# Optimization experiments

Measured on AMD Instinct MI355X. Metric: run time of the kernel, lower is better.

Reference implementation:

```python
import jax, jax.numpy as jnp
import numpy as np

D_MODEL = 2048
D_COMPARE = 2048
D_MEMORY = 2048
N_HEADS = 16
KV_HEADS = 4
KV_REPEAT = N_HEADS // KV_HEADS          # 4
C_HD = D_COMPARE // N_HEADS              # 128 compare head dim
M_HD = D_MEMORY // N_HEADS               # 128 memory head dim
TOTAL_OUT = D_COMPARE + KV_HEADS * C_HD + KV_HEADS * M_HD  # 3072


def setup_inputs() -> dict:
    key = jax.random.key(0)
    ks = jax.random.split(key, 5)
    b, t = 2, 2048
    x = jax.random.normal(ks[0], (b, t, D_MODEL), dtype=jnp.float32)
    s_in = 1.0 / np.sqrt(D_MODEL)
    s_out = 1.0 / np.sqrt(D_MEMORY)
    in_w = jax.random.uniform(ks[1], (TOTAL_OUT, D_MODEL), jnp.float32, -s_in, s_in)
    in_b = jax.random.uniform(ks[2], (TOTAL_OUT,), jnp.float32, -s_in, s_in)
    out_w = jax.random.uniform(ks[3], (D_MODEL, D_MEMORY), jnp.float32, -s_out, s_out)
    out_b = jax.random.uniform(ks[4], (D_MODEL,), jnp.float32, -s_out, s_out)
    return {"x": x, "in_w": in_w, "in_b": in_b, "out_w": out_w, "out_b": out_b}


def reference(x, in_w, in_b, out_w, out_b):
    b, t, _ = x.shape
    packed = jnp.einsum("btd,od->bto", x, in_w) + in_b          # [b,t,TOTAL_OUT]
    q, k, v = jnp.split(packed, [D_COMPARE, D_COMPARE + KV_HEADS * C_HD], axis=-1)
    # q: [b, kv, rep, t, hd] -- head h maps to kv group h // KV_REPEAT
    # (torch repeat_interleave on KV head dim == grouped reshape of q heads)
    q = q.reshape(b, t, KV_HEADS, KV_REPEAT, C_HD).transpose(0, 2, 3, 1, 4)
    k = k.reshape(b, t, KV_HEADS, C_HD).transpose(0, 2, 1, 3)   # [b,kv,t,hd]
    v = v.reshape(b, t, KV_HEADS, M_HD).transpose(0, 2, 1, 3)   # [b,kv,t,mhd]
    scale = 1.0 / np.sqrt(C_HD)
    scores = jnp.einsum("bgrqd,bgkd->bgrqk", q, k) * scale      # [b,kv,rep,t,t]
    attn = jax.nn.softmax(scores, axis=-1)
    y = jnp.einsum("bgrqk,bgkd->bgrqd", attn, v)                # [b,kv,rep,t,mhd]
    y = y.transpose(0, 3, 1, 2, 4).reshape(b, t, D_MEMORY)      # heads back in order
    return jnp.einsum("btm,dm->btd", y, out_w) + out_b
```

## Files before the change

kernel.cpp:

```cpp
#include <hip/hip_runtime.h>
#include <hip/hip_bf16.h>
#include <stdint.h>

#define DEV __device__ __forceinline__

typedef __attribute__((ext_vector_type(8))) short bf16x8;
typedef __attribute__((ext_vector_type(4))) float f32x4;
typedef __attribute__((ext_vector_type(16))) float f32x16;

DEV unsigned short f2bf(float f) {
  unsigned u = __builtin_bit_cast(unsigned, f);
  unsigned r = u + 0x7FFF + ((u >> 16) & 1);
  return (unsigned short)(r >> 16);
}

DEV unsigned short f2bfh(float f) {
  __bf16 h = (__bf16)f;
  return __builtin_bit_cast(unsigned short, h);
}

typedef __attribute__((address_space(1))) void gvoid;
typedef __attribute__((address_space(3))) void lvoid;

DEV void g2l16(const void* g, void* l) {
  __builtin_amdgcn_global_load_lds((gvoid*)g, (lvoid*)l, 16, 0, 0);
}

#define MFMA16(a, b, c) __builtin_amdgcn_mfma_f32_16x16x32_bf16(a, b, c, 0, 0, 0)
#define MFMA32(a, b, c) __builtin_amdgcn_mfma_f32_32x32x16_bf16(a, b, c, 0, 0, 0)

__global__ void k_cvt3(const float* __restrict__ x, unsigned short* __restrict__ xo, int nx4,
                       const float* __restrict__ w, unsigned short* __restrict__ wo, int nw4,
                       const float* __restrict__ v, unsigned short* __restrict__ vo, int nv4) {
  int i = blockIdx.x * blockDim.x + threadIdx.x;
  int stride = gridDim.x * blockDim.x;
  int tot = nx4 + nw4 + nv4;
  for (; i < tot; i += stride) {
    const float* src; unsigned short* dst; int j = i;
    if (j < nx4) { src = x; dst = xo; }
    else if ((j -= nx4) < nw4) { src = w; dst = wo; }
    else { j -= nw4; src = v; dst = vo; }
    float4 val = reinterpret_cast<const float4*>(src)[j];
    ushort4 o;
    o.x = f2bf(val.x); o.y = f2bf(val.y); o.z = f2bf(val.z); o.w = f2bf(val.w);
    reinterpret_cast<ushort4*>(dst)[j] = o;
  }
}

template<bool BF16OUT>
__global__ __launch_bounds__(256, 2) void k_gemm(
    const unsigned short* __restrict__ A, const unsigned short* __restrict__ B,
    const float* __restrict__ bias, void* __restrict__ C,
    int M, int N, int K) {
  __shared__ unsigned short As[128 * 32];
  __shared__ unsigned short Bs[128 * 32];
  int tid = threadIdx.x;
  int lane = tid & 63, wid = tid >> 6;
  int bm = blockIdx.y * 128, bn = blockIdx.x * 128;
  int wm = (wid >> 1) * 64, wn = (wid & 1) * 64;
  int row16 = lane & 15, kq = lane >> 4;
  f32x4 acc[4][4] = {};
  int r = tid >> 2, c = (tid & 3) * 8;
  const unsigned short* Ag = A + (size_t)(bm + r) * K + c;
  const unsigned short* Bg = B + (size_t)(bn + r) * K + c;
  for (int k0 = 0; k0 < K; k0 += 32) {
    g2l16(Ag + k0, &As[tid * 8]);
    g2l16(Ag + (size_t)64 * K + k0, &As[2048 + tid * 8]);
    g2l16(Bg + k0, &Bs[tid * 8]);
    g2l16(Bg + (size_t)64 * K + k0, &Bs[2048 + tid * 8]);
    __syncthreads();
    bf16x8 a[4], b[4];
#pragma unroll
    for (int m = 0; m < 4; m++) a[m] = *(const bf16x8*)&As[(wm + m * 16 + row16) * 32 + kq * 8];
#pragma unroll
    for (int n = 0; n < 4; n++) b[n] = *(const bf16x8*)&Bs[(wn + n * 16 + row16) * 32 + kq * 8];
    __builtin_amdgcn_s_setprio(1);
#pragma unroll
    for (int m = 0; m < 4; m++)
#pragma unroll
      for (int n = 0; n < 4; n++)
        acc[m][n] = MFMA16(a[m], b[n], acc[m][n]);
    __builtin_amdgcn_s_setprio(0);
    __syncthreads();
  }
#pragma unroll
  for (int n = 0; n < 4; n++) {
    int col = bn + wn + n * 16 + row16;
    float bv = bias[col];
#pragma unroll
    for (int m = 0; m < 4; m++) {
      int rw = bm + wm + m * 16 + kq * 4;
#pragma unroll
      for (int j = 0; j < 4; j++) {
        float v = acc[m][n][j] + bv;
        if (BF16OUT) ((unsigned short*)C)[(size_t)(rw + j) * N + col] = f2bf(v);
        else         ((float*)C)[(size_t)(rw + j) * N + col] = v;
      }
    }
  }
}

__global__ void k_vt(const unsigned short* __restrict__ packed, unsigned short* __restrict__ vT) {
  __shared__ unsigned short tile[64][136];
  int g = blockIdx.y;
  int b = g >> 2, kv = g & 3;
  int t0 = blockIdx.x * 64;
  int tid = threadIdx.x;
#pragma unroll
  for (int i = 0; i < 4; i++) {
    int tl = i * 16 + (tid >> 4);
    int d0 = (tid & 15) * 8;
    bf16x8 v = *(const bf16x8*)&packed[(size_t)(b * 2048 + t0 + tl) * 3072 + 2560 + kv * 128 + d0];
    *(bf16x8*)&tile[tl][d0] = v;
  }
  __syncthreads();
  int d = tid >> 1, ts = (tid & 1) * 32;
  size_t obase = (size_t)(g * 128 + d) * 2048 + t0 + ts;
#pragma unroll
  for (int j = 0; j < 4; j++) {
    bf16x8 o;
#pragma unroll
    for (int e = 0; e < 8; e++) o[e] = (short)tile[ts + j * 8 + e][d];
    *(bf16x8*)&vT[obase + j * 8] = o;
  }
}

__global__ __launch_bounds__(256, 2) void k_flash(
    const unsigned short* __restrict__ packed,
    const unsigned short* __restrict__ vT,
    unsigned short* __restrict__ Y) {
  __shared__ unsigned short Ks[2][64 * 128];
  __shared__ unsigned short Vs[128 * 64];
  __shared__ unsigned short Ps[4][32 * 64];
  __shared__ float Axc[4][32];
  int tid = threadIdx.x, lane = tid & 63, wid = tid >> 6;
  int l31 = lane & 31, hi = lane >> 5;
  int kx = l31 & 15;
  int vx = l31 & 7;
  int g = blockIdx.x;
  int s8 = g & 7;
  int b = s8 >> 2, kv = s8 & 3;
  int w = g >> 3;
  int h = kv * 4 + (w & 3);
  int qt = w >> 2;
  size_t prow = (size_t)b * 2048;

  unsigned short* Q = &Ks[0][0];
  {
    int rr = tid >> 4;
    int cc = ((tid & 15) ^ rr) * 8;
    const unsigned short* qg = packed + (prow + qt * 128 + rr) * 3072 + h * 128 + cc;
#pragma unroll
    for (int i = 0; i < 8; i++)
      g2l16(qg + (size_t)i * 16 * 3072, &Q[i * 2048 + tid * 8]);
  }
  asm volatile("s_waitcnt vmcnt(0)" ::: "memory");
  __builtin_amdgcn_s_barrier();
  bf16x8 q[8];
  int qrow = wid * 32 + l31;
#pragma unroll
  for (int kc = 0; kc < 8; kc++)
    q[kc] = *(const bf16x8*)&Q[qrow * 128 + (((2 * kc + hi) ^ kx) * 8)];
  asm volatile("s_waitcnt lgkmcnt(0)" ::: "memory");
  __builtin_amdgcn_sched_barrier(0);
  __builtin_amdgcn_s_barrier();

  const unsigned short* kg0 = packed + prow * 3072 + 2048 + kv * 128;
  const unsigned short* vg0 = vT + (size_t)(b * 4 + kv) * 128 * 2048;
  int krr = tid >> 4;
  int kcc = ((tid & 15) ^ krr) * 8;
  int vrr = tid >> 3;
  int vcc = ((tid & 7) ^ (vrr & 7)) * 8;

  auto stageK = [&](int t, int kbuf) {
    const unsigned short* kg = kg0 + (size_t)(t * 64 + krr) * 3072 + kcc;
#pragma unroll
    for (int i = 0; i < 4; i++)
      g2l16(kg + (size_t)i * 16 * 3072, &Ks[kbuf][i * 2048 + tid * 8]);
  };
  auto stageV = [&](int t) {
    const unsigned short* vg = vg0 + (size_t)vrr * 2048 + t * 64 + vcc;
#pragma unroll
    for (int i = 0; i < 4; i++)
      g2l16(vg + (size_t)i * 32 * 2048, &Vs[i * 2048 + tid * 8]);
  };

  stageK(0, 0);
  stageV(0);
  asm volatile("s_waitcnt vmcnt(4)" ::: "memory");
  __builtin_amdgcn_s_barrier();

  f32x16 o[4] = {};
  float mr = -1e30f, lr = 0.f;
  const float sc2 = 0.08838834764831845f * 1.4426950408889634f;

  for (int t = 0; t < 32; t++) {
    int kb = t & 1;
    int tn = t < 31 ? t + 1 : 31;

    f32x16 st[2] = {};
#pragma unroll
    for (int kb2 = 0; kb2 < 2; kb2++) {
      bf16x8 ak[8];
#pragma unroll
      for (int kc = 0; kc < 8; kc++)
        ak[kc] = *(const bf16x8*)&Ks[kb][(kb2 * 32 + l31) * 128 + (((2 * kc + hi) ^ kx) * 8)];
      __builtin_amdgcn_s_setprio(1);
#pragma unroll
      for (int kc = 0; kc < 8; kc++)
        st[kb2] = MFMA32(ak[kc], q[kc], st[kb2]);
      __builtin_amdgcn_s_setprio(0);
    }

    stageK(tn, kb ^ 1);

    float m0 = -1e30f, m1 = -1e30f;
#pragma unroll
    for (int r = 0; r < 16; r += 2) {
      m0 = fmaxf(m0, fmaxf(st[0][r], st[0][r + 1]));
      m1 = fmaxf(m1, fmaxf(st[1][r], st[1][r + 1]));
    }
    float p = fmaxf(m0, m1);
    p = fmaxf(p, __shfl_xor(p, 32));
    p *= sc2;
    if (!__all(p <= mr + 8.f)) {
      float mn = fmaxf(mr, p);
      float al = exp2f(mr - mn);
      mr = mn;
      lr *= al;
      Axc[wid][l31] = al;
      float alo[16];
#pragma unroll
      for (int r = 0; r < 16; r++)
        alo[r] = Axc[wid][(r & 3) + 8 * (r >> 2) + 4 * hi];
#pragma unroll
      for (int db = 0; db < 4; db++)
#pragma unroll
        for (int r = 0; r < 16; r++) o[db][r] *= alo[r];
    }
    float nm = -mr;
    float rs = 0.f;
#pragma unroll
    for (int kb2 = 0; kb2 < 2; kb2++) {
      float s[4];
#pragma unroll
      for (int u = 0; u < 4; u++) {
        st[kb2][4 * u + 0] = exp2f(fmaf(st[kb2][4 * u + 0], sc2, nm));
        st[kb2][4 * u + 1] = exp2f(fmaf(st[kb2][4 * u + 1], sc2, nm));
        st[kb2][4 * u + 2] = exp2f(fmaf(st[kb2][4 * u + 2], sc2, nm));
        st[kb2][4 * u + 3] = exp2f(fmaf(st[kb2][4 * u + 3], sc2, nm));
        s[u] = (st[kb2][4 * u + 0] + st[kb2][4 * u + 1]) +
               (st[kb2][4 * u + 2] + st[kb2][4 * u + 3]);
      }
      rs += (s[0] + s[1]) + (s[2] + s[3]);
    }
    rs += __shfl_xor(rs, 32);
    lr += rs;

#pragma unroll
    for (int kb2 = 0; kb2 < 2; kb2++)
#pragma unroll
      for (int u = 0; u < 4; u++) {
        ushort4 pw;
        pw.x = f2bfh(st[kb2][4 * u + 0]);
        pw.y = f2bfh(st[kb2][4 * u + 1]);
        pw.z = f2bfh(st[kb2][4 * u + 2]);
        pw.w = f2bfh(st[kb2][4 * u + 3]);
        *(ushort4*)&Ps[wid][l31 * 64 + (((u + 4 * kb2) ^ vx) * 8) + hi * 4] = pw;
      }
    bf16x8 pf[4];
#pragma unroll
    for (int ks = 0; ks < 4; ks++)
      pf[ks] = *(const bf16x8*)&Ps[wid][l31 * 64 + (((2 * ks + hi) ^ vx) * 8)];

    asm volatile("s_waitcnt vmcnt(4)" ::: "memory");
    __builtin_amdgcn_s_barrier();

#pragma unroll
    for (int db = 0; db < 4; db++) {
      bf16x8 bv[4];
#pragma unroll
      for (int ks = 0; ks < 4; ks++)
        bv[ks] = *(const bf16x8*)&Vs[(32 * db + l31) * 64 + (((2 * ks + hi) ^ vx) * 8)];
      __builtin_amdgcn_s_setprio(1);
#pragma unroll
      for (int ks = 0; ks < 4; ks++)
        o[db] = MFMA32(pf[ks], bv[ks], o[db]);
      __builtin_amdgcn_s_setprio(0);
    }

    __builtin_amdgcn_s_barrier();
    stageV(tn);
    asm volatile("s_waitcnt vmcnt(4)" ::: "memory");
    __builtin_amdgcn_s_barrier();
  }
  asm volatile("s_waitcnt vmcnt(0)" ::: "memory");

  Axc[wid][l31] = lr;
#pragma unroll
  for (int r = 0; r < 16; r++) {
    int ql = (r & 3) + 8 * (r >> 2) + 4 * hi;
    float inv = 1.f / Axc[wid][ql];
    size_t orow = prow + (size_t)qt * 128 + wid * 32 + ql;
#pragma unroll
    for (int db = 0; db < 4; db++)
      Y[orow * 2048 + h * 128 + db * 32 + l31] = f2bfh(o[db][r] * inv);
  }
}

extern "C" void kernel_launch(void* const* d_in, const int* in_sizes, int n_in,
                              void* d_out, int out_size, void* d_ws, size_t ws_size,
                              hipStream_t stream) {
  const float* x     = (const float*)d_in[0];
  const float* in_w  = (const float*)d_in[1];
  const float* in_b  = (const float*)d_in[2];
  const float* out_w = (const float*)d_in[3];
  const float* out_b = (const float*)d_in[4];
  float* out = (float*)d_out;

  unsigned short* xb     = (unsigned short*)d_ws;
  unsigned short* wb     = xb + 8388608;
  unsigned short* owb    = wb + 6291456;
  unsigned short* packed = owb + 4194304;
  unsigned short* vt     = packed + 12582912;
  unsigned short* y      = vt + 2097152;

  k_cvt3<<<dim3(2048), dim3(256), 0, stream>>>(x, xb, 8388608 / 4,
                                               in_w, wb, 6291456 / 4,
                                               out_w, owb, 4194304 / 4);

  k_gemm<true><<<dim3(24, 32), dim3(256), 0, stream>>>(xb, wb, in_b, packed, 4096, 3072, 2048);
  k_vt<<<dim3(32, 8), dim3(256), 0, stream>>>(packed, vt);
  k_flash<<<dim3(512), dim3(256), 0, stream>>>(packed, vt, y);
  k_gemm<false><<<dim3(16, 32), dim3(256), 0, stream>>>(y, owb, out_b, out, 4096, 2048, 2048);
}
```

Baseline: 225.2 us.

## Keep P in registers via permlane swap, double-buffer V, compute row sums with MFMA

The P matrix is converted to bf16 with packed converts and rearranged across lanes with v_permlane32_swap, so it no longer goes through an LDS round trip. V gets a second LDS buffer, and K and V for the next tile are both prefetched at the top of each iteration, which cuts the per-iteration barriers from three to one. Row sums are now accumulated by MFMA against a ones vector instead of scalar adds and shuffles. In exchange it uses more LDS and spends extra MFMA work on the sums, and the row sums now come from bf16-rounded P values.

```diff
diff --git a/kernel.cpp b/kernel.cpp
--- a/kernel.cpp
+++ b/kernel.cpp
@@ -7,6 +7,7 @@
 typedef __attribute__((ext_vector_type(8))) short bf16x8;
 typedef __attribute__((ext_vector_type(4))) float f32x4;
 typedef __attribute__((ext_vector_type(16))) float f32x16;
+typedef __attribute__((ext_vector_type(4))) unsigned u32x4;
 
 DEV unsigned short f2bf(float f) {
   unsigned u = __builtin_bit_cast(unsigned, f);
@@ -17,6 +18,16 @@
 DEV unsigned short f2bfh(float f) {
   __bf16 h = (__bf16)f;
   return __builtin_bit_cast(unsigned short, h);
+}
+
+DEV unsigned cvtpk(float lo, float hi) {
+  unsigned r;
+  asm("v_cvt_pk_bf16_f32 %0, %1, %2" : "=v"(r) : "v"(lo), "v"(hi));
+  return r;
+}
+
+DEV void plswap(unsigned &a, unsigned &b) {
+  asm("v_permlane32_swap_b32 %0, %1" : "+v"(a), "+v"(b));
 }
 
 typedef __attribute__((address_space(1))) void gvoid;
@@ -130,8 +141,7 @@
     const unsigned short* __restrict__ vT,
     unsigned short* __restrict__ Y) {
   __shared__ unsigned short Ks[2][64 * 128];
-  __shared__ unsigned short Vs[128 * 64];
-  __shared__ unsigned short Ps[4][32 * 64];
+  __shared__ unsigned short Vs[2][128 * 64];
   __shared__ float Axc[4][32];
   int tid = threadIdx.x, lane = tid & 63, wid = tid >> 6;
   int l31 = lane & 31, hi = lane >> 5;
@@ -172,31 +182,38 @@
   int vrr = tid >> 3;
   int vcc = ((tid & 7) ^ (vrr & 7)) * 8;
 
-  auto stageK = [&](int t, int kbuf) {
+  auto stageK = [&](int t, int buf) {
     const unsigned short* kg = kg0 + (size_t)(t * 64 + krr) * 3072 + kcc;
 #pragma unroll
     for (int i = 0; i < 4; i++)
-      g2l16(kg + (size_t)i * 16 * 3072, &Ks[kbuf][i * 2048 + tid * 8]);
+      g2l16(kg + (size_t)i * 16 * 3072, &Ks[buf][i * 2048 + tid * 8]);
   };
-  auto stageV = [&](int t) {
+  auto stageV = [&](int t, int buf) {
     const unsigned short* vg = vg0 + (size_t)vrr * 2048 + t * 64 + vcc;
 #pragma unroll
     for (int i = 0; i < 4; i++)
-      g2l16(vg + (size_t)i * 32 * 2048, &Vs[i * 2048 + tid * 8]);
+      g2l16(vg + (size_t)i * 32 * 2048, &Vs[buf][i * 2048 + tid * 8]);
   };
 
   stageK(0, 0);
-  stageV(0);
-  asm volatile("s_waitcnt vmcnt(4)" ::: "memory");
+  stageV(0, 0);
+  asm volatile("s_waitcnt vmcnt(0)" ::: "memory");
   __builtin_amdgcn_s_barrier();
 
   f32x16 o[4] = {};
-  float mr = -1e30f, lr = 0.f;
+  f32x16 ls = {};
+  float mr = -1e30f;
   const float sc2 = 0.08838834764831845f * 1.4426950408889634f;
+  bf16x8 ones;
+#pragma unroll
+  for (int e = 0; e < 8; e++) ones[e] = (short)0x3F80;
 
   for (int t = 0; t < 32; t++) {
-    int kb = t & 1;
+    int buf = t & 1;
     int tn = t < 31 ? t + 1 : 31;
+
+    stageK(tn, buf ^ 1);
+    stageV(tn, buf ^ 1);
 
     f32x16 st[2] = {};
 #pragma unroll
@@ -204,15 +221,13 @@
       bf16x8 ak[8];
 #pragma unroll
       for (int kc = 0; kc < 8; kc++)
-        ak[kc] = *(const bf16x8*)&Ks[kb][(kb2 * 32 + l31) * 128 + (((2 * kc + hi) ^ kx) * 8)];
+        ak[kc] = *(const bf16x8*)&Ks[buf][(kb2 * 32 + l31) * 128 + (((2 * kc + hi) ^ kx) * 8)];
       __builtin_amdgcn_s_setprio(1);
 #pragma unroll
       for (int kc = 0; kc < 8; kc++)
         st[kb2] = MFMA32(ak[kc], q[kc], st[kb2]);
       __builtin_amdgcn_s_setprio(0);
     }
-
-    stageK(tn, kb ^ 1);
 
     float m0 = -1e30f, m1 = -1e30f;
 #pragma unroll
@@ -227,7 +242,6 @@
       float mn = fmaxf(mr, p);
       float al = exp2f(mr - mn);
       mr = mn;
-      lr *= al;
       Axc[wid][l31] = al;
       float alo[16];
 #pragma unroll
@@ -237,70 +251,57 @@
       for (int db = 0; db < 4; db++)
 #pragma unroll
         for (int r = 0; r < 16; r++) o[db][r] *= alo[r];
+#pragma unroll
+      for (int r = 0; r < 16; r++) ls[r] *= alo[r];
     }
     float nm = -mr;
-    float rs = 0.f;
+#pragma unroll
+    for (int kb2 = 0; kb2 < 2; kb2++)
+#pragma unroll
+      for (int r = 0; r < 16; r++)
+        st[kb2][r] = exp2f(fmaf(st[kb2][r], sc2, nm));
+
+    bf16x8 pf[4];
 #pragma unroll
     for (int kb2 = 0; kb2 < 2; kb2++) {
-      float s[4];
-#pragma unroll
-      for (int u = 0; u < 4; u++) {
-        st[kb2][4 * u + 0] = exp2f(fmaf(st[kb2][4 * u + 0], sc2, nm));
-        st[kb2][4 * u + 1] = exp2f(fmaf(st[kb2][4 * u + 1], sc2, nm));
-        st[kb2][4 * u + 2] = exp2f(fmaf(st[kb2][4 * u + 2], sc2, nm));
-        st[kb2][4 * u + 3] = exp2f(fmaf(st[kb2][4 * u + 3], sc2, nm));
-        s[u] = (st[kb2][4 * u + 0] + st[kb2][4 * u + 1]) +
-               (st[kb2][4 * u + 2] + st[kb2][4 * u + 3]);
-      }
-      rs += (s[0] + s[1]) + (s[2] + s[3]);
-    }
-    rs += __shfl_xor(rs, 32);
-    lr += rs;
-
-#pragma unroll
-    for (int kb2 = 0; kb2 < 2; kb2++)
-#pragma unroll
-      for (int u = 0; u < 4; u++) {
-        ushort4 pw;
-        pw.x = f2bfh(st[kb2][4 * u + 0]);
-        pw.y = f2bfh(st[kb2][4 * u + 1]);
-        pw.z = f2bfh(st[kb2][4 * u + 2]);
-        pw.w = f2bfh(st[kb2][4 * u + 3]);
-        *(ushort4*)&Ps[wid][l31 * 64 + (((u + 4 * kb2) ^ vx) * 8) + hi * 4] = pw;
-      }
-    bf16x8 pf[4];
-#pragma unroll
-    for (int ks = 0; ks < 4; ks++)
-      pf[ks] = *(const bf16x8*)&Ps[wid][l31 * 64 + (((2 * ks + hi) ^ vx) * 8)];
-
-    asm volatile("s_waitcnt vmcnt(4)" ::: "memory");
-    __builtin_amdgcn_s_barrier();
+      unsigned E0 = cvtpk(st[kb2][0],  st[kb2][1]);
+      unsigned E1 = cvtpk(st[kb2][2],  st[kb2][3]);
+      unsigned E2 = cvtpk(st[kb2][4],  st[kb2][5]);
+      unsigned E3 = cvtpk(st[kb2][6],  st[kb2][7]);
+      unsigned E4 = cvtpk(st[kb2][8],  st[kb2][9]);
+      unsigned E5 = cvtpk(st[kb2][10], st[kb2][11]);
+      unsigned E6 = cvtpk(st[kb2][12], st[kb2][13]);
+      unsigned E7 = cvtpk(st[kb2][14], st[kb2][15]);
+      plswap(E0, E2); plswap(E1, E3);
+      plswap(E4, E6); plswap(E5, E7);
+      pf[2 * kb2 + 0] = __builtin_bit_cast(bf16x8, u32x4{E0, E1, E2, E3});
+      pf[2 * kb2 + 1] = __builtin_bit_cast(bf16x8, u32x4{E4, E5, E6, E7});
+    }
 
 #pragma unroll
     for (int db = 0; db < 4; db++) {
       bf16x8 bv[4];
 #pragma unroll
       for (int ks = 0; ks < 4; ks++)
-        bv[ks] = *(const bf16x8*)&Vs[(32 * db + l31) * 64 + (((2 * ks + hi) ^ vx) * 8)];
+        bv[ks] = *(const bf16x8*)&Vs[buf][(32 * db + l31) * 64 + (((2 * ks + hi) ^ vx) * 8)];
       __builtin_amdgcn_s_setprio(1);
 #pragma unroll
       for (int ks = 0; ks < 4; ks++)
         o[db] = MFMA32(pf[ks], bv[ks], o[db]);
       __builtin_amdgcn_s_setprio(0);
     }
-
+#pragma unroll
+    for (int ks = 0; ks < 4; ks++)
+      ls = MFMA32(pf[ks], ones, ls);
+
+    asm volatile("s_waitcnt vmcnt(0)" ::: "memory");
     __builtin_amdgcn_s_barrier();
-    stageV(tn);
-    asm volatile("s_waitcnt vmcnt(4)" ::: "memory");
-    __builtin_amdgcn_s_barrier();
-  }
-  asm volatile("s_waitcnt vmcnt(0)" ::: "memory");
-
-  Axc[wid][l31] = lr;
+  }
+
 #pragma unroll
   for (int r = 0; r < 16; r++) {
     int ql = (r & 3) + 8 * (r >> 2) + 4 * hi;
-    float inv = 1.f / Axc[wid][ql];
+    float inv = 1.f / ls[r];
     size_t orow = prow + (size_t)qt * 128 + wid * 32 + ql;
 #pragma unroll
     for (int db = 0; db < 4; db++)
```

After: 226.4 us. No clear change (+0.5%).
